# Kernel optimization log

Hardware: AMD Instinct MI355X
Metric: run time of the kernel (lower is better)

Reference implementation:

```python
import jax, jax.numpy as jnp
import numpy as np

B, S, D_IN, D_OUT, RANK = 4, 2048, 4096, 4096, 16
ALPHA = 16
SCALING = ALPHA / RANK  # 1.0


def setup_inputs() -> dict:
    key = jax.random.key(0)
    k_x, k_q, k_b, k_a, k_bb = jax.random.split(key, 5)
    x = jax.random.normal(k_x, (B, S, D_IN), dtype=jnp.float32)
    # int4 symmetric quantized weight values in [-8, 7], stored as int32
    qweight = jax.random.randint(k_q, (D_OUT, D_IN), -8, 8, dtype=jnp.int32)
    # per-tensor scale (abs_max / 7 in the original); a plausible small value
    scales = jnp.array([0.01], dtype=jnp.float32)
    bias = jax.random.normal(k_b, (D_OUT,), dtype=jnp.float32) * 0.02
    # LoRA params (acting as "trained" values; original inits A kaiming, B zeros)
    lora_A = jax.random.normal(k_a, (D_IN, RANK), dtype=jnp.float32) * (1.0 / np.sqrt(D_IN))
    lora_B = jax.random.normal(k_bb, (RANK, D_OUT), dtype=jnp.float32) * 0.01
    return {"x": x, "qweight": qweight, "scales": scales, "bias": bias,
            "lora_A": lora_A, "lora_B": lora_B}


def reference(x, qweight, scales, bias, lora_A, lora_B):
    # dequantize: int4 values * scalar scale -> fp32 weight [D_OUT, D_IN]
    w = qweight.astype(jnp.float32) * scales[0]
    # F.linear(x, w, bias): x @ w.T + bias
    out = jnp.einsum('bsd,od->bso', x, w) + bias
    # LoRA low-rank path: (x @ A) @ B * scaling (dropout=0 -> identity)
    lora_out = (x @ lora_A) @ lora_B
    return out + lora_out * SCALING
```

## Files before the change

### kernel.cpp

```cpp
#include <hip/hip_runtime.h>
#include <stdint.h>
#include <math.h>


static constexpr int Mdim = 8192;
static constexpr int Ndim = 4096;
static constexpr int Kdim = 4096;

typedef __bf16 bf16x8 __attribute__((ext_vector_type(8)));
typedef float f32x4 __attribute__((ext_vector_type(4)));
typedef int   i32x4 __attribute__((ext_vector_type(4)));

__device__ __forceinline__ void async_copy16(const void* gptr, void* lptr) {
    auto g = (const __attribute__((address_space(1))) unsigned char*)(uintptr_t)gptr;
    auto l = (__attribute__((address_space(3))) unsigned char*)(uintptr_t)lptr;
    __builtin_amdgcn_global_load_lds(g, l, 16, 0, 0);
}

static constexpr int BLK_W = Ndim * Kdim / (256 * 16);
static constexpr int BLK_X = Mdim;
static constexpr int BLK_BT = Ndim / 256;

__global__ void __launch_bounds__(256) prep_kernel(
        const float* __restrict__ x,
        const int* __restrict__ qw,
        const float* __restrict__ lA,
        const float* __restrict__ lB,
        int8_t* __restrict__ x_i8,
        int8_t* __restrict__ w_i8,
        int8_t* __restrict__ a_i8t,
        __bf16* __restrict__ Blbt,
        float* __restrict__ row_scale,
        float* __restrict__ a_scale_g) {
    __shared__ float red[8];
    int b = blockIdx.x;
    const int tid = threadIdx.x;

    if (b == 0) {
        float am = 0.f;
        const float4* ap = (const float4*)lA + tid * 64;
        for (int i = 0; i < 64; ++i) {
            float4 v = ap[i];
            am = fmaxf(am, fmaxf(fmaxf(fabsf(v.x), fabsf(v.y)),
                                 fmaxf(fabsf(v.z), fabsf(v.w))));
        }
        for (int off = 32; off; off >>= 1) am = fmaxf(am, __shfl_xor(am, off));
        if ((tid & 63) == 0) red[tid >> 6] = am;
        __syncthreads();
        if (tid == 0) {
            float m = fmaxf(fmaxf(red[0], red[1]), fmaxf(red[2], red[3]));
            red[4] = m;
            a_scale_g[0] = m > 0.f ? m / 127.f : 0.f;
        }
        __syncthreads();
        float amax = red[4];
        float inv = amax > 0.f ? 127.f / amax : 0.f;
        int k0 = tid * 16;
#pragma unroll
        for (int r = 0; r < 16; ++r) {
            int8_t o[16];
#pragma unroll
            for (int kk = 0; kk < 16; ++kk) {
                float v = lA[(size_t)(k0 + kk) * 16 + r];
                o[kk] = (int8_t)(int)rintf(v * inv);
            }
            *(i32x4*)(a_i8t + (size_t)r * Kdim + k0) = *(i32x4*)o;
        }
        return;
    }
    b -= 1;

    if (b < BLK_W) {
        size_t idx = ((size_t)b * 256 + tid) * 16;
        const int4* q = (const int4*)(qw + idx);
        int4 q0 = q[0], q1 = q[1], q2 = q[2], q3 = q[3];
        int8_t o[16] = {(int8_t)q0.x, (int8_t)q0.y, (int8_t)q0.z, (int8_t)q0.w,
                        (int8_t)q1.x, (int8_t)q1.y, (int8_t)q1.z, (int8_t)q1.w,
                        (int8_t)q2.x, (int8_t)q2.y, (int8_t)q2.z, (int8_t)q2.w,
                        (int8_t)q3.x, (int8_t)q3.y, (int8_t)q3.z, (int8_t)q3.w};
        *(i32x4*)(w_i8 + idx) = *(i32x4*)o;
        return;
    }
    b -= BLK_W;

    if (b < BLK_X) {
        const int row = b;
        const float4* xp = (const float4*)(x + (size_t)row * Kdim) + tid * 4;
        float4 v0 = xp[0], v1 = xp[1], v2 = xp[2], v3 = xp[3];
        float am = 0.f;
        am = fmaxf(am, fmaxf(fmaxf(fabsf(v0.x), fabsf(v0.y)), fmaxf(fabsf(v0.z), fabsf(v0.w))));
        am = fmaxf(am, fmaxf(fmaxf(fabsf(v1.x), fabsf(v1.y)), fmaxf(fabsf(v1.z), fabsf(v1.w))));
        am = fmaxf(am, fmaxf(fmaxf(fabsf(v2.x), fabsf(v2.y)), fmaxf(fabsf(v2.z), fabsf(v2.w))));
        am = fmaxf(am, fmaxf(fmaxf(fabsf(v3.x), fabsf(v3.y)), fmaxf(fabsf(v3.z), fabsf(v3.w))));
        for (int off = 32; off; off >>= 1) am = fmaxf(am, __shfl_xor(am, off));
        if ((tid & 63) == 0) red[tid >> 6] = am;
        __syncthreads();
        if (tid == 0) {
            float m = fmaxf(fmaxf(red[0], red[1]), fmaxf(red[2], red[3]));
            red[4] = m;
            row_scale[row] = m > 0.f ? m / 127.f : 0.f;
        }
        __syncthreads();
        float amax = red[4];
        float inv = amax > 0.f ? 127.f / amax : 0.f;
        float vv[16] = {v0.x, v0.y, v0.z, v0.w, v1.x, v1.y, v1.z, v1.w,
                        v2.x, v2.y, v2.z, v2.w, v3.x, v3.y, v3.z, v3.w};
        int8_t o[16];
#pragma unroll
        for (int i = 0; i < 16; ++i) o[i] = (int8_t)(int)rintf(vv[i] * inv);
        *(i32x4*)(x_i8 + (size_t)row * Kdim + tid * 16) = *(i32x4*)o;
        return;
    }
    b -= BLK_X;

    {
        int c = b * 256 + tid;
        __bf16 tmp[16];
#pragma unroll
        for (int r = 0; r < 16; ++r) tmp[r] = (__bf16)lB[(size_t)r * Ndim + c];
        *(bf16x8*)(Blbt + (size_t)c * 16) = *(bf16x8*)tmp;
        *(bf16x8*)(Blbt + (size_t)c * 16 + 8) = *(bf16x8*)(tmp + 8);
    }
}

__global__ void __launch_bounds__(256) xa_kernel(
        const int8_t* __restrict__ x_i8,
        const int8_t* __restrict__ a_i8t,
        const float* __restrict__ row_scale,
        const float* __restrict__ a_scale_g,
        __bf16* __restrict__ xab) {
    __shared__ __align__(16) char sX[64 * 64];
    __shared__ __align__(16) char sAq[16 * 64];
    const int tid = threadIdx.x, wave = tid >> 6, lane = tid & 63;
    const int quad = lane >> 4, l16 = lane & 15;
    const int bm = blockIdx.x;
    const size_t xbase = ((size_t)bm * 64 + (tid >> 2)) * Kdim + (tid & 3) * 16;
    i32x4 acc = {0, 0, 0, 0};
    for (int k0 = 0; k0 < Kdim; k0 += 64) {
        __syncthreads();
        async_copy16(x_i8 + xbase + k0, sX + tid * 16);
        if (tid < 64)
            async_copy16(a_i8t + (size_t)(tid >> 2) * Kdim + (tid & 3) * 16 + k0,
                         sAq + tid * 16);
        __syncthreads();
        i32x4 af = *(const i32x4*)(sX + (wave * 16 + l16) * 64 + quad * 16);
        i32x4 bf = *(const i32x4*)(sAq + l16 * 64 + quad * 16);
        acc = __builtin_amdgcn_mfma_i32_16x16x64_i8(af, bf, acc, 0, 0, 0);
    }
    const float asc = a_scale_g[0];
    const int rl = wave * 16 + quad * 4;
#pragma unroll
    for (int r = 0; r < 4; ++r) {
        int grow = bm * 64 + rl + r;
        float v = (float)acc[r] * row_scale[grow] * asc;
        xab[(size_t)grow * 16 + l16] = (__bf16)v;
    }
}

__global__ void __launch_bounds__(256) gemm_kernel(
        const int8_t* __restrict__ Xq,
        const int8_t* __restrict__ Wq,
        const float* __restrict__ scales,
        const float* __restrict__ bias,
        const float* __restrict__ row_scale,
        const __bf16* __restrict__ xab,
        const __bf16* __restrict__ Blbt,
        float* __restrict__ out) {
    __shared__ __align__(16) char smem[16384 + 512];
    char* sA = smem;
    char* sB = smem + 8192;

    const int tid = threadIdx.x, wave = tid >> 6, lane = tid & 63;
    const int wm = wave >> 1, wn = wave & 1;
    const int quad = lane >> 4, l16 = lane & 15;
    const int bm = blockIdx.y, bn = blockIdx.x;

    const int arow = tid >> 2;
    const int acolb = (tid & 3) * 16;
    const size_t a_base = (size_t)(bm * 128 + arow) * Kdim + acolb;
    const size_t b_base = (size_t)(bn * 128 + arow) * Kdim + acolb;

    i32x4 acc[4][4];
#pragma unroll
    for (int i = 0; i < 4; ++i)
#pragma unroll
        for (int j = 0; j < 4; ++j) acc[i][j] = i32x4{0, 0, 0, 0};

    for (int k0 = 0; k0 < Kdim; k0 += 64) {
        __syncthreads();
        async_copy16(Xq + a_base + k0,                     sA + tid * 16);
        async_copy16(Xq + a_base + (size_t)64 * Kdim + k0, sA + 4096 + tid * 16);
        async_copy16(Wq + b_base + k0,                     sB + tid * 16);
        async_copy16(Wq + b_base + (size_t)64 * Kdim + k0, sB + 4096 + tid * 16);
        __syncthreads();

        i32x4 aF[4], bF[4];
#pragma unroll
        for (int i = 0; i < 4; ++i)
            aF[i] = *(const i32x4*)(sA + (wm * 64 + i * 16 + l16) * 64 + quad * 16);
#pragma unroll
        for (int j = 0; j < 4; ++j)
            bF[j] = *(const i32x4*)(sB + (wn * 64 + j * 16 + l16) * 64 + quad * 16);

#pragma unroll
        for (int i = 0; i < 4; ++i)
#pragma unroll
            for (int j = 0; j < 4; ++j)
                acc[i][j] = __builtin_amdgcn_mfma_i32_16x16x64_i8(aF[i], bF[j], acc[i][j], 0, 0, 0);
    }

    const float wsc = scales[0];
    float bj4[4];
#pragma unroll
    for (int j = 0; j < 4; ++j) bj4[j] = bias[bn * 128 + wn * 64 + j * 16 + l16];

    __syncthreads();
    async_copy16((const char*)(xab + (size_t)bm * 128 * 16) + tid * 16, smem + tid * 16);
    async_copy16((const char*)(Blbt + (size_t)bn * 128 * 16) + tid * 16, smem + 4096 + tid * 16);
    if (tid < 32)
        async_copy16((const char*)(row_scale + bm * 128) + tid * 16, smem + 8192 + tid * 16);
    __syncthreads();

    const __bf16* sXA = (const __bf16*)smem;
    const __bf16* sBL = (const __bf16*)(smem + 4096);
    const float*  sRS = (const float*)(smem + 8192);

    bf16x8 zf;
#pragma unroll
    for (int k = 0; k < 8; ++k) zf[k] = (__bf16)0.f;

    bf16x8 aF2[4], bF2[4];
#pragma unroll
    for (int i = 0; i < 4; ++i) {
        if (quad < 2) aF2[i] = *(const bf16x8*)(sXA + (wm * 64 + i * 16 + l16) * 16 + quad * 8);
        else          aF2[i] = zf;
    }
#pragma unroll
    for (int j = 0; j < 4; ++j) {
        if (quad < 2) bF2[j] = *(const bf16x8*)(sBL + (wn * 64 + j * 16 + l16) * 16 + quad * 8);
        else          bF2[j] = zf;
    }

    f32x4 lacc[4][4];
#pragma unroll
    for (int j = 0; j < 4; ++j)
#pragma unroll
        for (int i = 0; i < 4; ++i)
            lacc[i][j] = f32x4{bj4[j], bj4[j], bj4[j], bj4[j]};

#pragma unroll
    for (int i = 0; i < 4; ++i)
#pragma unroll
        for (int j = 0; j < 4; ++j)
            lacc[i][j] = __builtin_amdgcn_mfma_f32_16x16x32_bf16(aF2[i], bF2[j], lacc[i][j], 0, 0, 0);

    const int col0 = bn * 128 + wn * 64 + l16;
    const int rl0 = wm * 64 + quad * 4;
#pragma unroll
    for (int j = 0; j < 4; ++j) {
        const int col = col0 + j * 16;
#pragma unroll
        for (int i = 0; i < 4; ++i) {
            const int lr = rl0 + i * 16;
#pragma unroll
            for (int r = 0; r < 4; ++r) {
                float sx = sRS[lr + r] * wsc;
                out[(size_t)(bm * 128 + lr + r) * Ndim + col] =
                    (float)acc[i][j][r] * sx + lacc[i][j][r];
            }
        }
    }
}

extern "C" void kernel_launch(void* const* d_in, const int* in_sizes, int n_in,
                              void* d_out, int out_size, void* d_ws, size_t ws_size,
                              hipStream_t stream) {
    const float* x      = (const float*)d_in[0];
    const int*   qw     = (const int*)d_in[1];
    const float* scales = (const float*)d_in[2];
    const float* bias   = (const float*)d_in[3];
    const float* lA     = (const float*)d_in[4];
    const float* lB     = (const float*)d_in[5];
    float* out = (float*)d_out;

    char* ws = (char*)d_ws;
    int8_t* x_i8   = (int8_t*)ws;
    int8_t* w_i8   = (int8_t*)(ws + 33554432);
    int8_t* a_i8t  = (int8_t*)(ws + 50331648);
    __bf16* xab    = (__bf16*)(ws + 50397184);
    __bf16* Blbt   = (__bf16*)(ws + 50659328);
    float* row_scale = (float*)(ws + 50790400);
    float* a_scale_g = (float*)(ws + 50823168);

    const int prep_blocks = 1 + BLK_W + BLK_X + BLK_BT;
    prep_kernel<<<prep_blocks, 256, 0, stream>>>(
        x, qw, lA, lB, x_i8, w_i8, a_i8t, Blbt, row_scale, a_scale_g);
    xa_kernel<<<Mdim / 64, 256, 0, stream>>>(x_i8, a_i8t, row_scale, a_scale_g, xab);
    dim3 grid(Ndim / 128, Mdim / 128);
    gemm_kernel<<<grid, 256, 0, stream>>>(x_i8, w_i8, scales, bias, row_scale,
                                          xab, Blbt, out);
}
```

Before: 476.4 us.

## Double-buffer int8 GEMM and LoRA xA loads, XCD-swizzle tiles, split-K xA

The main int8 GEMM now double-buffers its LDS tiles, so the async global-to-LDS copy for the next K step overlaps the MFMA work on the current one. This halves the barriers per iteration. Its shared-memory layout becomes chunk-major (k-chunk by row) to cut bank conflicts on fragment reads. Block IDs are remapped so each XCD works on a contiguous 16x16 tile region, which should improve L2 reuse. The small x@A kernel is split four ways along K with fp32 atomicAdd into a buffer that the prep kernel zeroes, and is double-buffered too. This adds atomics and twice the LDS in exchange for more parallelism.

```diff
diff --git a/kernel.cpp b/kernel.cpp
--- a/kernel.cpp
+++ b/kernel.cpp
@@ -31,7 +31,8 @@
         int8_t* __restrict__ a_i8t,
         __bf16* __restrict__ Blbt,
         float* __restrict__ row_scale,
-        float* __restrict__ a_scale_g) {
+        float* __restrict__ a_scale_g,
+        float* __restrict__ xabf) {
     __shared__ float red[8];
     int b = blockIdx.x;
     const int tid = threadIdx.x;
@@ -120,6 +121,10 @@
         for (int r = 0; r < 16; ++r) tmp[r] = (__bf16)lB[(size_t)r * Ndim + c];
         *(bf16x8*)(Blbt + (size_t)c * 16) = *(bf16x8*)tmp;
         *(bf16x8*)(Blbt + (size_t)c * 16 + 8) = *(bf16x8*)(tmp + 8);
+        f32x4 z = {0.f, 0.f, 0.f, 0.f};
+        f32x4* zp = (f32x4*)(xabf + (size_t)(b * 256 + tid) * 32);
+#pragma unroll
+        for (int i = 0; i < 8; ++i) zp[i] = z;
     }
 }
 
@@ -128,24 +133,37 @@
         const int8_t* __restrict__ a_i8t,
         const float* __restrict__ row_scale,
         const float* __restrict__ a_scale_g,
-        __bf16* __restrict__ xab) {
-    __shared__ __align__(16) char sX[64 * 64];
-    __shared__ __align__(16) char sAq[16 * 64];
+        float* __restrict__ xabf) {
+    __shared__ __align__(16) char sX[2][4096];
+    __shared__ __align__(16) char sAq[2][1024];
     const int tid = threadIdx.x, wave = tid >> 6, lane = tid & 63;
     const int quad = lane >> 4, l16 = lane & 15;
-    const int bm = blockIdx.x;
-    const size_t xbase = ((size_t)bm * 64 + (tid >> 2)) * Kdim + (tid & 3) * 16;
+    const int bm = blockIdx.x >> 2;
+    const int kc = blockIdx.x & 3;
+    const int kbeg = kc * (Kdim / 4);
+
+    const size_t xoff = (size_t)(bm * 64 + (tid & 63)) * Kdim + (tid >> 6) * 16;
+    const size_t aoff = (size_t)(tid & 15) * Kdim + (tid >> 4) * 16;
+
     i32x4 acc = {0, 0, 0, 0};
-    for (int k0 = 0; k0 < Kdim; k0 += 64) {
-        __syncthreads();
-        async_copy16(x_i8 + xbase + k0, sX + tid * 16);
-        if (tid < 64)
-            async_copy16(a_i8t + (size_t)(tid >> 2) * Kdim + (tid & 3) * 16 + k0,
-                         sAq + tid * 16);
-        __syncthreads();
-        i32x4 af = *(const i32x4*)(sX + (wave * 16 + l16) * 64 + quad * 16);
-        i32x4 bf = *(const i32x4*)(sAq + l16 * 64 + quad * 16);
+    async_copy16(x_i8 + xoff + kbeg, sX[0] + tid * 16);
+    if (tid < 64) async_copy16(a_i8t + aoff + kbeg, sAq[0] + tid * 16);
+    __syncthreads();
+    int cur = 0;
+    const int rdA = (quad * 64 + wave * 16 + l16) * 16;
+    const int rdB = (quad * 16 + l16) * 16;
+#pragma unroll 1
+    for (int t = 0; t < 16; ++t) {
+        if (t < 15) {
+            async_copy16(x_i8 + xoff + kbeg + (t + 1) * 64, sX[cur ^ 1] + tid * 16);
+            if (tid < 64)
+                async_copy16(a_i8t + aoff + kbeg + (t + 1) * 64, sAq[cur ^ 1] + tid * 16);
+        }
+        i32x4 af = *(const i32x4*)(sX[cur] + rdA);
+        i32x4 bf = *(const i32x4*)(sAq[cur] + rdB);
         acc = __builtin_amdgcn_mfma_i32_16x16x64_i8(af, bf, acc, 0, 0, 0);
+        __syncthreads();
+        cur ^= 1;
     }
     const float asc = a_scale_g[0];
     const int rl = wave * 16 + quad * 4;
@@ -153,7 +171,7 @@
     for (int r = 0; r < 4; ++r) {
         int grow = bm * 64 + rl + r;
         float v = (float)acc[r] * row_scale[grow] * asc;
-        xab[(size_t)grow * 16 + l16] = (__bf16)v;
+        atomicAdd(xabf + (size_t)grow * 16 + l16, v);
     }
 }
 
@@ -163,22 +181,31 @@
         const float* __restrict__ scales,
         const float* __restrict__ bias,
         const float* __restrict__ row_scale,
-        const __bf16* __restrict__ xab,
+        const float* __restrict__ xabf,
         const __bf16* __restrict__ Blbt,
         float* __restrict__ out) {
-    __shared__ __align__(16) char smem[16384 + 512];
-    char* sA = smem;
-    char* sB = smem + 8192;
+    __shared__ __align__(16) char smem[32768];
 
     const int tid = threadIdx.x, wave = tid >> 6, lane = tid & 63;
     const int wm = wave >> 1, wn = wave & 1;
     const int quad = lane >> 4, l16 = lane & 15;
-    const int bm = blockIdx.y, bn = blockIdx.x;
-
-    const int arow = tid >> 2;
-    const int acolb = (tid & 3) * 16;
-    const size_t a_base = (size_t)(bm * 128 + arow) * Kdim + acolb;
-    const size_t b_base = (size_t)(bn * 128 + arow) * Kdim + acolb;
+
+    const int bid = blockIdx.y * gridDim.x + blockIdx.x;
+    const int xcd = bid & 7;
+    const int local = bid >> 3;
+    const int bm = (xcd >> 1) * 16 + (local >> 4);
+    const int bn = (xcd & 1) * 16 + (local & 15);
+
+    const int srow = tid & 127;
+    const int sq = tid >> 7;
+    const size_t a_off0 = (size_t)(bm * 128 + srow) * Kdim + sq * 16;
+    const size_t a_off1 = a_off0 + 32;
+    const size_t b_off0 = (size_t)(bn * 128 + srow) * Kdim + sq * 16;
+    const size_t b_off1 = b_off0 + 32;
+    const int dst0 = tid * 16, dst1 = 4096 + tid * 16;
+
+    const int aoffL = quad * 2048 + (wm * 64 + l16) * 16;
+    const int boffL = quad * 2048 + (wn * 64 + l16) * 16;
 
     i32x4 acc[4][4];
 #pragma unroll
@@ -186,27 +213,40 @@
 #pragma unroll
         for (int j = 0; j < 4; ++j) acc[i][j] = i32x4{0, 0, 0, 0};
 
-    for (int k0 = 0; k0 < Kdim; k0 += 64) {
-        __syncthreads();
-        async_copy16(Xq + a_base + k0,                     sA + tid * 16);
-        async_copy16(Xq + a_base + (size_t)64 * Kdim + k0, sA + 4096 + tid * 16);
-        async_copy16(Wq + b_base + k0,                     sB + tid * 16);
-        async_copy16(Wq + b_base + (size_t)64 * Kdim + k0, sB + 4096 + tid * 16);
-        __syncthreads();
-
+    auto stage = [&](int k0, char* PA, char* PB) {
+        async_copy16(Xq + a_off0 + k0, PA + dst0);
+        async_copy16(Xq + a_off1 + k0, PA + dst1);
+        async_copy16(Wq + b_off0 + k0, PB + dst0);
+        async_copy16(Wq + b_off1 + k0, PB + dst1);
+    };
+    auto compute = [&](const char* PA, const char* PB) {
         i32x4 aF[4], bF[4];
 #pragma unroll
-        for (int i = 0; i < 4; ++i)
-            aF[i] = *(const i32x4*)(sA + (wm * 64 + i * 16 + l16) * 64 + quad * 16);
-#pragma unroll
-        for (int j = 0; j < 4; ++j)
-            bF[j] = *(const i32x4*)(sB + (wn * 64 + j * 16 + l16) * 64 + quad * 16);
-
+        for (int i = 0; i < 4; ++i) aF[i] = *(const i32x4*)(PA + aoffL + i * 256);
+#pragma unroll
+        for (int j = 0; j < 4; ++j) bF[j] = *(const i32x4*)(PB + boffL + j * 256);
 #pragma unroll
         for (int i = 0; i < 4; ++i)
 #pragma unroll
             for (int j = 0; j < 4; ++j)
                 acc[i][j] = __builtin_amdgcn_mfma_i32_16x16x64_i8(aF[i], bF[j], acc[i][j], 0, 0, 0);
+    };
+
+    stage(0, smem, smem + 8192);
+    __syncthreads();
+    int cur = 0;
+#pragma unroll 1
+    for (int t = 0; t < 63; ++t) {
+        char* nxt = smem + ((cur ^ 1) << 14);
+        stage((t + 1) * 64, nxt, nxt + 8192);
+        char* c = smem + (cur << 14);
+        compute(c, c + 8192);
+        __syncthreads();
+        cur ^= 1;
+    }
+    {
+        char* c = smem + (cur << 14);
+        compute(c, c + 8192);
     }
 
     const float wsc = scales[0];
@@ -215,15 +255,19 @@
     for (int j = 0; j < 4; ++j) bj4[j] = bias[bn * 128 + wn * 64 + j * 16 + l16];
 
     __syncthreads();
-    async_copy16((const char*)(xab + (size_t)bm * 128 * 16) + tid * 16, smem + tid * 16);
-    async_copy16((const char*)(Blbt + (size_t)bn * 128 * 16) + tid * 16, smem + 4096 + tid * 16);
+    async_copy16((const char*)xabf + (size_t)bm * 128 * 64 + tid * 16, smem + tid * 16);
+    async_copy16((const char*)xabf + (size_t)bm * 128 * 64 + 4096 + tid * 16,
+                 smem + 4096 + tid * 16);
+    async_copy16((const char*)(Blbt + (size_t)bn * 128 * 16) + tid * 16,
+                 smem + 8192 + tid * 16);
     if (tid < 32)
-        async_copy16((const char*)(row_scale + bm * 128) + tid * 16, smem + 8192 + tid * 16);
+        async_copy16((const char*)(row_scale + bm * 128) + tid * 16,
+                     smem + 12288 + tid * 16);
     __syncthreads();
 
-    const __bf16* sXA = (const __bf16*)smem;
-    const __bf16* sBL = (const __bf16*)(smem + 4096);
-    const float*  sRS = (const float*)(smem + 8192);
+    const float*  sXAf = (const float*)smem;
+    const __bf16* sBL  = (const __bf16*)(smem + 8192);
+    const float*  sRS  = (const float*)(smem + 12288);
 
     bf16x8 zf;
 #pragma unroll
@@ -232,8 +276,19 @@
     bf16x8 aF2[4], bF2[4];
 #pragma unroll
     for (int i = 0; i < 4; ++i) {
-        if (quad < 2) aF2[i] = *(const bf16x8*)(sXA + (wm * 64 + i * 16 + l16) * 16 + quad * 8);
-        else          aF2[i] = zf;
+        if (quad < 2) {
+            const float* p = sXAf + (wm * 64 + i * 16 + l16) * 16 + quad * 8;
+            f32x4 u0 = *(const f32x4*)p;
+            f32x4 u1 = *(const f32x4*)(p + 4);
+            bf16x8 t;
+            t[0] = (__bf16)u0[0]; t[1] = (__bf16)u0[1];
+            t[2] = (__bf16)u0[2]; t[3] = (__bf16)u0[3];
+            t[4] = (__bf16)u1[0]; t[5] = (__bf16)u1[1];
+            t[6] = (__bf16)u1[2]; t[7] = (__bf16)u1[3];
+            aF2[i] = t;
+        } else {
+            aF2[i] = zf;
+        }
     }
 #pragma unroll
     for (int j = 0; j < 4; ++j) {
@@ -284,19 +339,19 @@
     float* out = (float*)d_out;
 
     char* ws = (char*)d_ws;
-    int8_t* x_i8   = (int8_t*)ws;
-    int8_t* w_i8   = (int8_t*)(ws + 33554432);
-    int8_t* a_i8t  = (int8_t*)(ws + 50331648);
-    __bf16* xab    = (__bf16*)(ws + 50397184);
-    __bf16* Blbt   = (__bf16*)(ws + 50659328);
-    float* row_scale = (float*)(ws + 50790400);
-    float* a_scale_g = (float*)(ws + 50823168);
+    int8_t* x_i8     = (int8_t*)ws;
+    int8_t* w_i8     = (int8_t*)(ws + 33554432);
+    int8_t* a_i8t    = (int8_t*)(ws + 50331648);
+    float*  xabf     = (float*)(ws + 50397184);
+    __bf16* Blbt     = (__bf16*)(ws + 50921472);
+    float*  row_scale = (float*)(ws + 51052544);
+    float*  a_scale_g = (float*)(ws + 51085312);
 
     const int prep_blocks = 1 + BLK_W + BLK_X + BLK_BT;
     prep_kernel<<<prep_blocks, 256, 0, stream>>>(
-        x, qw, lA, lB, x_i8, w_i8, a_i8t, Blbt, row_scale, a_scale_g);
-    xa_kernel<<<Mdim / 64, 256, 0, stream>>>(x_i8, a_i8t, row_scale, a_scale_g, xab);
+        x, qw, lA, lB, x_i8, w_i8, a_i8t, Blbt, row_scale, a_scale_g, xabf);
+    xa_kernel<<<512, 256, 0, stream>>>(x_i8, a_i8t, row_scale, a_scale_g, xabf);
     dim3 grid(Ndim / 128, Mdim / 128);
     gemm_kernel<<<grid, 256, 0, stream>>>(x_i8, w_i8, scales, bias, row_scale,
-                                          xab, Blbt, out);
-}
+                                          xabf, Blbt, out);
+}
```

Result: slower. 553.2 us (+16.1%).
